# Performance work log

Measured on AMD Instinct MI355X. Metric: run time of the kernel, lower is better.

## Reference

```python
import jax, jax.numpy as jnp
import numpy as np

B, S, D = 4, 2048, 768      # batch, seq_len, embedding_dim
I = 1536                    # inner_dim = embedding_dim * up_proj_factor
H, HD = 8, 64               # num_heads, head_dim
EPS = 1e-5


def setup_inputs() -> dict:
    key = jax.random.key(0)
    ks = jax.random.split(key, 12)
    std = 0.02
    f32 = jnp.float32
    p = {}
    p["x"] = jax.random.normal(ks[0], (B, S, D), f32)
    # block LayerNorm
    p["ln_g"] = jnp.ones((D,), f32)
    p["ln_b"] = jnp.zeros((D,), f32)
    # up / down projections (bias-free, as in the module)
    p["W_up"] = jax.random.normal(ks[1], (D, I), f32) * std
    p["W_down"] = jax.random.normal(ks[2], (I, D), f32) * std
    # mLSTM cell: q/k/v projections to num_heads*head_dim
    p["Wq"] = jax.random.normal(ks[3], (I, H * HD), f32) * std
    p["Wk"] = jax.random.normal(ks[4], (I, H * HD), f32) * std
    p["Wv"] = jax.random.normal(ks[5], (I, H * HD), f32) * std
    # scalar per-head input / forget gate pre-activations
    p["Wi"] = jax.random.normal(ks[6], (I, H), f32) * std
    p["bi"] = jnp.zeros((H,), f32)
    p["Wf"] = jax.random.normal(ks[7], (I, H), f32) * std
    p["bf"] = 3.0 * jnp.ones((H,), f32)  # positive forget-gate bias init
    # output gate and cell output projection
    p["Wo"] = jax.random.normal(ks[8], (I, H * HD), f32) * std
    p["bo"] = jnp.zeros((H * HD,), f32)
    p["mh_g"] = jnp.ones((H, HD), f32)  # per-head norm scale (group norm)
    p["W_out"] = jax.random.normal(ks[9], (H * HD, I), f32) * std
    return p


def _forward(x, ln_g, ln_b, W_up, Wq, Wk, Wv, Wi, bi, Wf, bf, Wo, bo, mh_g, W_out, W_down):
    resid = x
    # LayerNorm
    mu = x.mean(-1, keepdims=True)
    var = ((x - mu) ** 2).mean(-1, keepdims=True)
    h = (x - mu) * jax.lax.rsqrt(var + EPS) * ln_g + ln_b
    # up projection
    u = h @ W_up                                    # (B,S,I)
    # mLSTM projections
    q = (u @ Wq).reshape(B, S, H, HD)
    k = (u @ Wk).reshape(B, S, H, HD) * (HD ** -0.5)
    v = (u @ Wv).reshape(B, S, H, HD)
    i_raw = u @ Wi + bi                             # (B,S,H)
    f_raw = u @ Wf + bf                             # (B,S,H)

    def step(carry, inp):
        C, n, m = carry                             # C:(B,H,HD,HD) n:(B,H,HD) m:(B,H)
        qt, kt, vt, it, ft = inp
        # log-space stabilization of exponential gates
        m_new = jnp.maximum(ft + m, it)
        ig = jnp.exp(it - m_new)
        fg = jnp.exp(ft + m - m_new)
        C = fg[..., None, None] * C + ig[..., None, None] * (vt[..., :, None] * kt[..., None, :])
        n = fg[..., None] * n + ig[..., None] * kt
        num = jnp.einsum('bhvk,bhk->bhv', C, qt)
        den = jnp.maximum(jnp.abs(jnp.einsum('bhk,bhk->bh', n, qt)), 1.0)
        return (C, n, m_new), num / den[..., None]

    xs = (jnp.moveaxis(q, 1, 0), jnp.moveaxis(k, 1, 0), jnp.moveaxis(v, 1, 0),
          jnp.moveaxis(i_raw, 1, 0), jnp.moveaxis(f_raw, 1, 0))
    C0 = jnp.zeros((B, H, HD, HD), x.dtype)
    n0 = jnp.zeros((B, H, HD), x.dtype)
    m0 = jnp.zeros((B, H), x.dtype)
    _, hts = jax.lax.scan(step, (C0, n0, m0), xs)   # (S,B,H,HD)
    ht = jnp.moveaxis(hts, 0, 1)                    # (B,S,H,HD)
    # per-head normalization (group norm, scale only)
    mu2 = ht.mean(-1, keepdims=True)
    var2 = ((ht - mu2) ** 2).mean(-1, keepdims=True)
    hn = (ht - mu2) * jax.lax.rsqrt(var2 + EPS) * mh_g
    # output gate + cell output projection
    o = jax.nn.sigmoid(u @ Wo + bo).reshape(B, S, H, HD)
    y = (o * hn).reshape(B, S, H * HD) @ W_out      # (B,S,I)
    # down projection + residual (dropout=0 -> identity)
    return resid + y @ W_down


def reference(x, ln_g, ln_b, W_up, Wq, Wk, Wv, Wi, bi, Wf, bf, Wo, bo, mh_g, W_out, W_down):
    return _forward(x, ln_g, ln_b, W_up, Wq, Wk, Wv, Wi, bi, Wf, bf, Wo, bo, mh_g, W_out, W_down)
```

## Files before the change

kernel.cpp:

```cpp
#include <hip/hip_runtime.h>
#include <hip/hip_bf16.h>
#include <stdint.h>
#include <stddef.h>

typedef __bf16 bf16_t;
typedef __bf16 bf16x4 __attribute__((ext_vector_type(4)));
typedef __bf16 bf16x8 __attribute__((ext_vector_type(8)));
typedef float  f32x4  __attribute__((ext_vector_type(4)));

#define Bsz  4
#define Ssz  2048
#define Dsz  768
#define Isz  1536
#define Hn   8
#define HDsz 64
#define NTOK (Bsz*Ssz)
#define Lc   64
#define NCH  (Ssz/Lc)
#define NBH  (Bsz*Hn)

#define OFF_H      ((size_t)0)
#define OFF_WQX    ((size_t)12582912)
#define OFF_WQC    ((size_t)18874368)
#define OFF_WDOWNT ((size_t)22020096)
#define OFF_WOC    ((size_t)24379392)
#define OFF_WUPB   ((size_t)25165824)
#define OFF_WUIF   ((size_t)27525120)
#define OFF_BIAS   ((size_t)27549696)
#define OFF_WOUTB  ((size_t)27553792)
#define OFF_QKVO   ((size_t)29126656)
#define OFF_KT     ((size_t)62681088)
#define OFF_VT     ((size_t)71069696)
#define OFF_GATED  ((size_t)79458304)
#define OFF_G      ((size_t)87846912)
#define OFF_IFB    ((size_t)96235520)
#define OFF_BLOC   ((size_t)96759808)
#define OFF_MHAT   ((size_t)97021952)
#define OFF_MST    ((size_t)97284096)
#define OFF_DEC    ((size_t)97288192)
#define OFF_MEND   ((size_t)97292288)
#define OFF_NG     ((size_t)97296384)
#define OFF_NST    ((size_t)97558528)
#define OFF_WOCP   OFF_H
#define OFF_CSTB   OFF_H
#define OFF_COMPP  OFF_QKVO

__device__ __forceinline__ void gload16(const void* gsrc, void* ldst) {
  __builtin_amdgcn_global_load_lds(
      (const __attribute__((address_space(1))) void*)gsrc,
      (__attribute__((address_space(3))) void*)ldst, 16, 0, 0);
}

__device__ __forceinline__ float blockReduceSum256(float v) {
  #pragma unroll
  for (int o = 1; o < 64; o <<= 1) v += __shfl_xor(v, o, 64);
  __shared__ float sh[4];
  int wid = threadIdx.x >> 6;
  __syncthreads();
  if ((threadIdx.x & 63) == 0) sh[wid] = v;
  __syncthreads();
  return sh[0] + sh[1] + sh[2] + sh[3];
}

__global__ __launch_bounds__(256) void prep_weights(
    const float* __restrict__ W_up, const float* __restrict__ Wq,
    const float* __restrict__ Wk, const float* __restrict__ Wv,
    const float* __restrict__ Wo, const float* __restrict__ W_down,
    const float* __restrict__ W_out, const float* __restrict__ bo,
    const float* __restrict__ bi, const float* __restrict__ bfv,
    bf16_t* __restrict__ wqxT, bf16_t* __restrict__ wdownT,
    bf16_t* __restrict__ woutB, bf16_t* __restrict__ wupB,
    float* __restrict__ biasA) {
  __shared__ float tile[32][33];
  const int bid = blockIdx.x;
  const int tx = threadIdx.x, ty = threadIdx.y;
  const float* src; bf16_t* dst; int K, N, bx, by; float scale = 1.f;
  if (bid < 768)       { int l = bid;        src = Wq;     dst = wqxT;                      K = 1536; N = 512; bx = l % 16; by = l / 16; }
  else if (bid < 1536) { int l = bid - 768;  src = Wk;     dst = wqxT + (size_t)512 * Isz;  K = 1536; N = 512; bx = l % 16; by = l / 16; scale = 0.125f; }
  else if (bid < 2304) { int l = bid - 1536; src = Wv;     dst = wqxT + (size_t)1024 * Isz; K = 1536; N = 512; bx = l % 16; by = l / 16; }
  else if (bid < 3072) { int l = bid - 2304; src = Wo;     dst = wqxT + (size_t)1536 * Isz; K = 1536; N = 512; bx = l % 16; by = l / 16; }
  else if (bid < 4224) { int l = bid - 3072; src = W_down; dst = wdownT;                    K = 1536; N = 768; bx = l % 24; by = l / 24; }
  else if (bid < 4992) {
    int base = (bid - 4224) * 1024 + (ty * 32 + tx) * 4;
    #pragma unroll
    for (int e = 0; e < 4; ++e) woutB[base + e] = (bf16_t)W_out[base + e];
    return;
  } else if (bid < 6144) {
    int base = (bid - 4992) * 1024 + (ty * 32 + tx) * 4;
    #pragma unroll
    for (int e = 0; e < 4; ++e) wupB[base + e] = (bf16_t)W_up[base + e];
    return;
  } else {
    int tid = ty * 32 + tx;
    for (int i = tid; i < 528; i += 256)
      biasA[i] = (i < 512) ? bo[i] : ((i < 520) ? bi[i - 512] : bfv[i - 520]);
    return;
  }
  int n0 = bx * 32, k0 = by * 32;
  #pragma unroll
  for (int j = 0; j < 32; j += 8)
    tile[ty + j][tx] = src[(size_t)(k0 + ty + j) * N + n0 + tx];
  __syncthreads();
  #pragma unroll
  for (int j = 0; j < 32; j += 8)
    dst[(size_t)(n0 + ty + j) * K + k0 + tx] = (bf16_t)(tile[tx][ty + j] * scale);
}

__global__ __launch_bounds__(64) void build_wuif(const float* __restrict__ W_up,
                                                 const float* __restrict__ Wi,
                                                 const float* __restrict__ Wf,
                                                 bf16_t* __restrict__ dst ) {
  int d = blockIdx.x;
  int lane = threadIdx.x;
  float acc[16];
  #pragma unroll
  for (int j = 0; j < 16; ++j) acc[j] = 0.f;
  for (int i = lane; i < Isz; i += 64) {
    float w = W_up[(size_t)d * Isz + i];
    f32x4 wi0 = *(const f32x4*)&Wi[(size_t)i * 8];
    f32x4 wi1 = *(const f32x4*)&Wi[(size_t)i * 8 + 4];
    f32x4 wf0 = *(const f32x4*)&Wf[(size_t)i * 8];
    f32x4 wf1 = *(const f32x4*)&Wf[(size_t)i * 8 + 4];
    #pragma unroll
    for (int j = 0; j < 4; ++j) {
      acc[j]      += w * wi0[j];
      acc[4 + j]  += w * wi1[j];
      acc[8 + j]  += w * wf0[j];
      acc[12 + j] += w * wf1[j];
    }
  }
  #pragma unroll
  for (int j = 0; j < 16; ++j)
    #pragma unroll
    for (int o = 1; o < 64; o <<= 1) acc[j] += __shfl_xor(acc[j], o, 64);
  if (lane == 0) {
    #pragma unroll
    for (int j = 0; j < 16; ++j)
      dst[(size_t)j * Dsz + d] = (bf16_t)acc[j];
  }
}

__global__ __launch_bounds__(256) void gemm_partk(const bf16_t* __restrict__ A,
                                                  const bf16_t* __restrict__ Bt,
                                                  float* __restrict__ P,
                                                  int M, int N, int Ktot, int kslice) {
  __shared__ bf16_t As[128 * 64];
  __shared__ bf16_t Bs[128 * 64];
  const int t = threadIdx.x;
  const int w = t >> 6, l = t & 63;
  const int tile_m = blockIdx.y * 128, tile_n = blockIdx.x * 128;
  const int kz = blockIdx.z;
  const int wr = w >> 1, wc = w & 1;
  const int lrow = l >> 3;
  const int lks = ((l & 7) * 8) ^ (lrow << 3);
  const int l15 = l & 15, l4 = l >> 4;

  f32x4 acc[4][4];
  #pragma unroll
  for (int m = 0; m < 4; ++m)
    #pragma unroll
    for (int n = 0; n < 4; ++n) acc[m][n] = (f32x4){0.f, 0.f, 0.f, 0.f};

  for (int k0 = kz * kslice; k0 < kz * kslice + kslice; k0 += 64) {
    #pragma unroll
    for (int i = 0; i < 4; ++i) {
      int ch = w * 4 + i;
      int row = ch * 8 + lrow;
      gload16(A  + (size_t)(tile_m + row) * Ktot + k0 + lks, &As[ch * 512]);
      gload16(Bt + (size_t)(tile_n + row) * Ktot + k0 + lks, &Bs[ch * 512]);
    }
    __syncthreads();
    #pragma unroll
    for (int kk = 0; kk < 2; ++kk) {
      bf16x8 af[4], bfr[4];
      #pragma unroll
      for (int m = 0; m < 4; ++m) {
        int r = wr * 64 + m * 16 + l15;
        af[m] = *(const bf16x8*)&As[r * 64 + ((kk * 32 + l4 * 8) ^ ((r & 7) << 3))];
      }
      #pragma unroll
      for (int n = 0; n < 4; ++n) {
        int r = wc * 64 + n * 16 + l15;
        bfr[n] = *(const bf16x8*)&Bs[r * 64 + ((kk * 32 + l4 * 8) ^ ((r & 7) << 3))];
      }
      #pragma unroll
      for (int m = 0; m < 4; ++m)
        #pragma unroll
        for (int n = 0; n < 4; ++n)
          acc[m][n] = __builtin_amdgcn_mfma_f32_16x16x32_bf16(af[m], bfr[n], acc[m][n], 0, 0, 0);
    }
    __syncthreads();
  }

  const int rbase = tile_m + wr * 64 + l4 * 4;
  const int cbase = tile_n + wc * 64 + l15;
  float* Pz = P + (size_t)kz * M * N;
  #pragma unroll
  for (int m = 0; m < 4; ++m)
    #pragma unroll
    for (int n = 0; n < 4; ++n)
      #pragma unroll
      for (int j = 0; j < 4; ++j)
        Pz[(size_t)(rbase + m * 16 + j) * N + cbase + n * 16] = acc[m][n][j];
}

__global__ __launch_bounds__(256) void partk_reduce(const float* __restrict__ P,
                                                    bf16_t* __restrict__ out,
                                                    int nelem, int nz) {
  int i = blockIdx.x * 256 + threadIdx.x;
  if (i < nelem) {
    float s = 0.f;
    for (int z = 0; z < nz; ++z) s += P[(size_t)z * nelem + i];
    out[i] = (bf16_t)s;
  }
}

__global__ __launch_bounds__(256) void ln_kernel(const float* __restrict__ x,
                                                 const float* __restrict__ g,
                                                 const float* __restrict__ bta,
                                                 bf16_t* __restrict__ h) {
  size_t tok = blockIdx.x;
  const float* xr = x + tok * Dsz;
  int t = threadIdx.x;
  float v[3]; float s = 0.f;
  #pragma unroll
  for (int i = 0; i < 3; ++i) { v[i] = xr[t + 256 * i]; s += v[i]; }
  s = blockReduceSum256(s);
  float mu = s * (1.f / Dsz);
  float s2 = 0.f;
  #pragma unroll
  for (int i = 0; i < 3; ++i) { float d = v[i] - mu; s2 += d * d; }
  s2 = blockReduceSum256(s2);
  float rs = rsqrtf(s2 * (1.f / Dsz) + 1e-5f);
  #pragma unroll
  for (int i = 0; i < 3; ++i) {
    int col = t + 256 * i;
    h[tok * Dsz + col] = (bf16_t)((v[i] - mu) * rs * g[col] + bta[col]);
  }
}

__global__ __launch_bounds__(256) void ifproj_mfma(const bf16_t* __restrict__ h,
                                                   const bf16_t* __restrict__ wuifT,
                                                   const float* __restrict__ bi,
                                                   const float* __restrict__ bfv,
                                                   float* __restrict__ ifb) {
  __shared__ bf16_t As[128 * 64];
  __shared__ bf16_t Bs[16 * 64];
  const int t = threadIdx.x, w = t >> 6, l = t & 63;
  const int l15 = l & 15, l4 = l >> 4;
  const int lrow = l >> 3, lk = (l & 7) * 8;
  const int tile_m = blockIdx.x * 128;
  f32x4 acc[2];
  acc[0] = (f32x4){0.f, 0.f, 0.f, 0.f};
  acc[1] = (f32x4){0.f, 0.f, 0.f, 0.f};

  for (int k0 = 0; k0 < Dsz; k0 += 64) {
    #pragma unroll
    for (int i = 0; i < 4; ++i) {
      int ch = w * 4 + i;
      int row = ch * 8 + lrow;
      gload16(h + (size_t)(tile_m + row) * Dsz + k0 + lk, &As[ch * 512]);
    }
    if (t < 128) {
      int rr = t >> 3, c0 = (t & 7) * 8;
      *(bf16x8*)&Bs[rr * 64 + c0] = *(const bf16x8*)(wuifT + (size_t)rr * Dsz + k0 + c0);
    }
    __syncthreads();
    #pragma unroll
    for (int kk = 0; kk < 2; ++kk) {
      bf16x8 bfr = *(const bf16x8*)&Bs[l15 * 64 + kk * 32 + l4 * 8];
      #pragma unroll
      for (int m = 0; m < 2; ++m) {
        bf16x8 af = *(const bf16x8*)&As[(w * 32 + m * 16 + l15) * 64 + kk * 32 + l4 * 8];
        acc[m] = __builtin_amdgcn_mfma_f32_16x16x32_bf16(af, bfr, acc[m], 0, 0, 0);
      }
    }
    __syncthreads();
  }
  float bias = (l15 < 8) ? bi[l15] : bfv[l15 - 8];
  #pragma unroll
  for (int m = 0; m < 2; ++m)
    #pragma unroll
    for (int j = 0; j < 4; ++j) {
      int row = tile_m + w * 32 + m * 16 + l4 * 4 + j;
      ifb[(size_t)row * 16 + l15] = acc[m][j] + bias;
    }
}

template<int EPI>
__global__ __launch_bounds__(512, 4) void gemm_mn(const bf16_t* __restrict__ A,
                                                  const bf16_t* __restrict__ Bt,
                                                  void* __restrict__ Cout,
                                                  const void* __restrict__ extra,
                                                  bf16_t* __restrict__ kTg,
                                                  bf16_t* __restrict__ vTg,
                                                  int M, int N, int K) {
  __shared__ bf16_t As[256 * 64];
  __shared__ bf16_t Bs[128 * 64];
  const int t = threadIdx.x;
  const int w = t >> 6, l = t & 63;
  const int wm = w >> 1, wn = w & 1;
  const int l15 = l & 15, l4 = l >> 4;

  const int gx = gridDim.x;
  const int nwg = gx * gridDim.y;
  const int cpx = nwg >> 3;
  int bid = blockIdx.y * gx + blockIdx.x;
  int wg = (bid & 7) * cpx + (bid >> 3);
  const int tile_m = (wg / gx) * 256;
  const int tile_n = (wg % gx) * 128;

  f32x4 acc[4][4];
  #pragma unroll
  for (int m = 0; m < 4; ++m)
    #pragma unroll
    for (int n = 0; n < 4; ++n) acc[m][n] = (f32x4){0.f, 0.f, 0.f, 0.f};

  for (int k0 = 0; k0 < K; k0 += 64) {
    #pragma unroll
    for (int j = 0; j < 4; ++j) {
      int c = t + j * 512;
      int row = c >> 3;
      int ec = ((c & 7) * 8) ^ ((row & 7) << 3);
      gload16(A + (size_t)(tile_m + row) * K + k0 + ec, (char*)As + (size_t)c * 16);
    }
    #pragma unroll
    for (int j = 0; j < 2; ++j) {
      int c = t + j * 512;
      int row = c >> 3;
      int ec = ((c & 7) * 8) ^ ((row & 7) << 3);
      gload16(Bt + (size_t)(tile_n + row) * K + k0 + ec, (char*)Bs + (size_t)c * 16);
    }
    __syncthreads();
    #pragma unroll
    for (int kk = 0; kk < 2; ++kk) {
      bf16x8 aF[4], bF[4];
      #pragma unroll
      for (int m = 0; m < 4; ++m) {
        int r = wm * 64 + m * 16 + l15;
        aF[m] = *(const bf16x8*)((const char*)As + r * 128 + ((kk * 64 + l4 * 16) ^ ((r & 7) << 4)));
      }
      #pragma unroll
      for (int n = 0; n < 4; ++n) {
        int r = wn * 64 + n * 16 + l15;
        bF[n] = *(const bf16x8*)((const char*)Bs + r * 128 + ((kk * 64 + l4 * 16) ^ ((r & 7) << 4)));
      }
      #pragma unroll
      for (int m = 0; m < 4; ++m)
        #pragma unroll
        for (int n = 0; n < 4; ++n)
          acc[m][n] = __builtin_amdgcn_mfma_f32_16x16x32_bf16(aF[m], bF[n], acc[m][n], 0, 0, 0);
    }
    __syncthreads();
  }

  const int rbase = tile_m + wm * 64 + l4 * 4;
  const int cbase = tile_n + wn * 64 + l15;
  if constexpr (EPI == 5) {
    const float* bias = (const float*)extra;
    #pragma unroll
    for (int m = 0; m < 4; ++m) {
      int row0 = rbase + m * 16;
      int bb = row0 >> 11, s0 = row0 & 2047;
      #pragma unroll
      for (int n = 0; n < 4; ++n) {
        int col = cbase + n * 16;
        if (col < 512) {
          #pragma unroll
          for (int j = 0; j < 4; ++j)
            ((bf16_t*)Cout)[(size_t)(row0 + j) * 2048 + col] = (bf16_t)acc[m][n][j];
        } else if (col < 1024) {
          int hd = col - 512;
          bf16x4 pk;
          #pragma unroll
          for (int j = 0; j < 4; ++j) {
            bf16_t bv = (bf16_t)acc[m][n][j];
            ((bf16_t*)Cout)[(size_t)(row0 + j) * 2048 + col] = bv;
            pk[j] = bv;
          }
          *(bf16x4*)(kTg + ((size_t)(bb * 8 + (hd >> 6)) * 64 + (hd & 63)) * Ssz + s0) = pk;
        } else if (col < 1536) {
          int hd = col - 1024;
          bf16x4 pv;
          #pragma unroll
          for (int j = 0; j < 4; ++j) pv[j] = (bf16_t)acc[m][n][j];
          *(bf16x4*)(vTg + ((size_t)(bb * 8 + (hd >> 6)) * 64 + (hd & 63)) * Ssz + s0) = pv;
        } else {
          float b = bias[col - 1536];
          #pragma unroll
          for (int j = 0; j < 4; ++j) {
            float z = acc[m][n][j] + b;
            ((bf16_t*)Cout)[(size_t)(row0 + j) * 2048 + col] = (bf16_t)(1.f / (1.f + __expf(-z)));
          }
        }
      }
    }
  } else {
    #pragma unroll
    for (int m = 0; m < 4; ++m)
      #pragma unroll
      for (int n = 0; n < 4; ++n)
        #pragma unroll
        for (int j = 0; j < 4; ++j) {
          int row = rbase + m * 16 + j;
          int col = cbase + n * 16;
          ((float*)Cout)[(size_t)row * N + col] =
              acc[m][n][j] + ((const float*)extra)[(size_t)row * N + col];
        }
  }
}

__global__ __launch_bounds__(64) void gates_a(const float* __restrict__ ifb,
                                              float* __restrict__ blocal,
                                              float* __restrict__ Mhat) {
  int bh = blockIdx.x >> 5, c = blockIdx.x & 31;
  int b = bh >> 3, h = bh & 7;
  int lane = threadIdx.x;
  size_t tok = (size_t)b * Ssz + c * Lc + lane;
  float iv = ifb[tok * 16 + h];
  float fv = ifb[tok * 16 + 8 + h];
  float bt = fv;
  #pragma unroll
  for (int d = 1; d < 64; d <<= 1) { float o = __shfl_up(bt, d, 64); if (lane >= d) bt += o; }
  float a = iv - bt;
  float pm = a;
  #pragma unroll
  for (int d = 1; d < 64; d <<= 1) { float o = __shfl_up(pm, d, 64); if (lane >= d) pm = fmaxf(pm, o); }
  blocal[(size_t)bh * Ssz + c * Lc + lane] = bt;
  Mhat[(size_t)bh * Ssz + c * Lc + lane] = bt + pm;
}

__global__ void gates_b(const float* __restrict__ blocal, const float* __restrict__ Mhat,
                        float* __restrict__ mstart, float* __restrict__ decays,
                        float* __restrict__ mend) {
  int bh = threadIdx.x;
  if (bh < NBH) {
    float M = 0.f;
    for (int c = 0; c < NCH; ++c) {
      mstart[bh * NCH + c] = M;
      float bL = blocal[(size_t)bh * Ssz + c * Lc + 63];
      float Mh = Mhat[(size_t)bh * Ssz + c * Lc + 63];
      float Mn = fmaxf(M + bL, Mh);
      decays[bh * NCH + c] = __expf(M + bL - Mn);
      mend[bh * NCH + c] = Mn;
      M = Mn;
    }
  }
}

__global__ __launch_bounds__(256) void chunk_inc_mfma(const bf16_t* __restrict__ kTg,
                                                      const bf16_t* __restrict__ vTg,
                                                      const float* __restrict__ ifb,
                                                      const float* __restrict__ blocal,
                                                      const float* __restrict__ mend,
                                                      bf16_t* __restrict__ G,
                                                      float* __restrict__ ng) {
  int bh = blockIdx.x >> 5, c = blockIdx.x & 31;
  int b = bh >> 3, h = bh & 7;
  __shared__ bf16_t Vt[64 * 64];
  __shared__ bf16_t Kw[64 * 64];
  __shared__ float wsh[64];
  const int t = threadIdx.x, w = t >> 6, l = t & 63;
  const int l15 = l & 15, l4 = l >> 4;
  if (t < 64) {
    float mL = mend[bh * NCH + c];
    float bL = blocal[(size_t)bh * Ssz + c * Lc + 63];
    float bt = blocal[(size_t)bh * Ssz + c * Lc + t];
    float iv = ifb[((size_t)b * Ssz + c * Lc + t) * 16 + h];
    wsh[t] = __expf(iv + bL - bt - mL);
  }
  __syncthreads();
  {
    const int r = l >> 3, c8 = (l & 7) * 8;
    #pragma unroll
    for (int i = 0; i < 2; ++i) {
      int seg = w * 2 + i, row = seg * 8 + r;
      gload16(vTg + ((size_t)bh * 64 + row) * Ssz + c * 64 + c8, &Vt[seg * 512]);
    }
    #pragma unroll
    for (int i = 0; i < 2; ++i) {
      int e = t + i * 256; int row = e >> 3, c0 = (e & 7) * 8;
      bf16x8 kv = *(const bf16x8*)(kTg + ((size_t)bh * 64 + row) * Ssz + c * 64 + c0);
      #pragma unroll
      for (int j = 0; j < 8; ++j) kv[j] = (bf16_t)((float)kv[j] * wsh[c0 + j]);
      *(bf16x8*)&Kw[row * 64 + c0] = kv;
    }
  }
  __syncthreads();
  f32x4 acc[4];
  #pragma unroll
  for (int n = 0; n < 4; ++n) acc[n] = (f32x4){0.f, 0.f, 0.f, 0.f};
  #pragma unroll
  for (int kk = 0; kk < 2; ++kk) {
    bf16x8 af = *(const bf16x8*)&Vt[(w * 16 + l15) * 64 + kk * 32 + l4 * 8];
    #pragma unroll
    for (int n = 0; n < 4; ++n) {
      bf16x8 bfr = *(const bf16x8*)&Kw[(n * 16 + l15) * 64 + kk * 32 + l4 * 8];
      acc[n] = __builtin_amdgcn_mfma_f32_16x16x32_bf16(af, bfr, acc[n], 0, 0, 0);
    }
  }
  size_t gb = ((size_t)bh * NCH + c) * 4096;
  #pragma unroll
  for (int n = 0; n < 4; ++n)
    #pragma unroll
    for (int j = 0; j < 4; ++j) {
      int row = w * 16 + l4 * 4 + j;
      int col = n * 16 + l15;
      G[gb + (size_t)row * 64 + col] = (bf16_t)acc[n][j];
    }
  if (t < 64) {
    float s = 0.f;
    for (int s2 = 0; s2 < 64; ++s2) s += (float)Kw[t * 64 + s2];
    ng[((size_t)bh * NCH + c) * 64 + t] = s;
  }
}

__global__ __launch_bounds__(256) void state_scan(const bf16_t* __restrict__ G,
                                                  const float* __restrict__ ng,
                                                  const float* __restrict__ decays,
                                                  bf16_t* __restrict__ CstB,
                                                  float* __restrict__ nst) {
  int gid = blockIdx.x;
  if (gid < 512) {
    int idx = gid * 256 + threadIdx.x;
    int bh = idx >> 12, e = idx & 4095;
    const float* d = decays + bh * NCH;
    float C = 0.f;
    #pragma unroll
    for (int c = 0; c < NCH; ++c) {
      size_t o = ((size_t)bh * NCH + c) * 4096 + e;
      CstB[o] = (bf16_t)C;
      C = d[c] * C + (float)G[o];
    }
  } else {
    int idx = (gid - 512) * 256 + threadIdx.x;
    int bh = idx >> 6, e = idx & 63;
    const float* d = decays + bh * NCH;
    float n = 0.f;
    #pragma unroll
    for (int c = 0; c < NCH; ++c) {
      size_t o = ((size_t)bh * NCH + c) * 64 + e;
      nst[o] = n;
      n = d[c] * n + ng[o];
    }
  }
}

__global__ __launch_bounds__(256) void intra_mfma(const bf16_t* __restrict__ qkvo,
                                                  const bf16_t* __restrict__ vTg,
                                                  const bf16_t* __restrict__ CstB,
                                                  const float* __restrict__ nst,
                                                  const float* __restrict__ ifb,
                                                  const float* __restrict__ blocal,
                                                  const float* __restrict__ Mhat,
                                                  const float* __restrict__ mstart,
                                                  const float* __restrict__ mhg,
                                                  bf16_t* __restrict__ gated) {
  int bh = blockIdx.x >> 5, c = blockIdx.x & 31;
  int b = bh >> 3, h = bh & 7;
  __shared__ bf16_t qs[64 * 64];
  __shared__ bf16_t ks[64 * 64];
  __shared__ bf16_t vTs[64 * 64];
  __shared__ bf16_t Cs[64 * 64];
  __shared__ float nin[64], den_s[64], ssrc[64], sdst[64], esc[64];
  const int t = threadIdx.x, w = t >> 6, l = t & 63;
  const int l15 = l & 15, l4 = l >> 4;
  const size_t tok0 = (size_t)b * Ssz + c * Lc;
  const size_t cbase = ((size_t)bh * NCH + c) * 4096;

  if (t < 64) {
    nin[t] = nst[((size_t)bh * NCH + c) * 64 + t];
    float bt = blocal[(size_t)bh * Ssz + c * Lc + t];
    float Mh2 = Mhat[(size_t)bh * Ssz + c * Lc + t];
    float Mc = mstart[bh * NCH + c];
    float iv = ifb[(tok0 + t) * 16 + h];
    float mt = fmaxf(Mc + bt, Mh2);
    ssrc[t] = iv - bt;
    sdst[t] = bt - mt;
    esc[t]  = __expf(Mc + bt - mt);
  }
  {
    const int r = l >> 3, c8 = (l & 7) * 8;
    #pragma unroll
    for (int i = 0; i < 2; ++i) {
      int seg = w * 2 + i, row = seg * 8 + r;
      gload16(qkvo + (tok0 + row) * 2048 + h * 64 + c8,          &qs[seg * 512]);
      gload16(qkvo + (tok0 + row) * 2048 + 512 + h * 64 + c8,    &ks[seg * 512]);
      gload16(vTg + ((size_t)bh * 64 + row) * Ssz + c * 64 + c8, &vTs[seg * 512]);
      gload16(CstB + cbase + seg * 512 + l * 8,                  &Cs[seg * 512]);
    }
  }
  __syncthreads();

  f32x4 aS[4];
  #pragma unroll
  for (int n = 0; n < 4; ++n) aS[n] = (f32x4){0.f, 0.f, 0.f, 0.f};
  #pragma unroll
  for (int kk = 0; kk < 2; ++kk) {
    bf16x8 af = *(const bf16x8*)&qs[(w * 16 + l15) * 64 + kk * 32 + l4 * 8];
    #pragma unroll
    for (int n = 0; n < 4; ++n) {
      bf16x8 bfr = *(const bf16x8*)&ks[(n * 16 + l15) * 64 + kk * 32 + l4 * 8];
      aS[n] = __builtin_amdgcn_mfma_f32_16x16x32_bf16(af, bfr, aS[n], 0, 0, 0);
    }
  }
  {
    int row = w * 16 + (l >> 2);
    int c0 = (l & 3) * 16;
    float e = esc[row];
    #pragma unroll
    for (int i2 = 0; i2 < 2; ++i2) {
      bf16x8 v8 = *(const bf16x8*)&qs[row * 64 + c0 + i2 * 8];
      #pragma unroll
      for (int j = 0; j < 8; ++j) v8[j] = (bf16_t)((float)v8[j] * e);
      *(bf16x8*)&qs[row * 64 + c0 + i2 * 8] = v8;
    }
  }
  float rs[4] = {0.f, 0.f, 0.f, 0.f};
  #pragma unroll
  for (int n = 0; n < 4; ++n) {
    int col = n * 16 + l15;
    float es = ssrc[col];
    #pragma unroll
    for (int j = 0; j < 4; ++j) {
      int row = w * 16 + l4 * 4 + j;
      float p = (col <= row) ? aS[n][j] * __expf(es + sdst[row]) : 0.f;
      aS[n][j] = p;
      rs[j] += p;
    }
  }
  #pragma unroll
  for (int j = 0; j < 4; ++j) {
    rs[j] += __shfl_xor(rs[j], 1, 64);
    rs[j] += __shfl_xor(rs[j], 2, 64);
    rs[j] += __shfl_xor(rs[j], 4, 64);
    rs[j] += __shfl_xor(rs[j], 8, 64);
  }
  if (l15 == 0) {
    #pragma unroll
    for (int j = 0; j < 4; ++j) den_s[w * 16 + l4 * 4 + j] = rs[j];
  }
  __syncthreads();

  #pragma unroll
  for (int n = 0; n < 4; ++n)
    #pragma unroll
    for (int j = 0; j < 4; ++j)
      ks[(w * 16 + l4 * 4 + j) * 64 + n * 16 + l15] = (bf16_t)aS[n][j];

  {
    int row = w * 16 + (l >> 2);
    int c0 = (l & 3) * 16;
    float part = 0.f;
    #pragma unroll
    for (int i2 = 0; i2 < 16; ++i2)
      part += (float)qs[row * 64 + c0 + i2] * nin[c0 + i2];
    part += __shfl_xor(part, 1, 64);
    part += __shfl_xor(part, 2, 64);
    if ((l & 3) == 0)
      den_s[row] = fmaxf(fabsf(den_s[row] + part), 1.0f);
  }
  __syncthreads();

  f32x4 aO[4];
  #pragma unroll
  for (int n = 0; n < 4; ++n) aO[n] = (f32x4){0.f, 0.f, 0.f, 0.f};
  #pragma unroll
  for (int kk = 0; kk < 2; ++kk) {
    bf16x8 afP = *(const bf16x8*)&ks[(w * 16 + l15) * 64 + kk * 32 + l4 * 8];
    bf16x8 afQ = *(const bf16x8*)&qs[(w * 16 + l15) * 64 + kk * 32 + l4 * 8];
    #pragma unroll
    for (int n = 0; n < 4; ++n) {
      bf16x8 bV = *(const bf16x8*)&vTs[(n * 16 + l15) * 64 + kk * 32 + l4 * 8];
      bf16x8 bC = *(const bf16x8*)&Cs[(n * 16 + l15) * 64 + kk * 32 + l4 * 8];
      aO[n] = __builtin_amdgcn_mfma_f32_16x16x32_bf16(afP, bV, aO[n], 0, 0, 0);
      aO[n] = __builtin_amdgcn_mfma_f32_16x16x32_bf16(afQ, bC, aO[n], 0, 0, 0);
    }
  }

  #pragma unroll
  for (int j = 0; j < 4; ++j) {
    int row = w * 16 + l4 * 4 + j;
    float rinv = 1.f / den_s[row];
    float ov[4];
    #pragma unroll
    for (int n = 0; n < 4; ++n) ov[n] = aO[n][j] * rinv;
    float s = ov[0] + ov[1] + ov[2] + ov[3];
    s += __shfl_xor(s, 1, 64); s += __shfl_xor(s, 2, 64);
    s += __shfl_xor(s, 4, 64); s += __shfl_xor(s, 8, 64);
    float mu = s * (1.f / 64.f);
    float s2 = 0.f;
    #pragma unroll
    for (int n = 0; n < 4; ++n) { float d = ov[n] - mu; s2 += d * d; }
    s2 += __shfl_xor(s2, 1, 64); s2 += __shfl_xor(s2, 2, 64);
    s2 += __shfl_xor(s2, 4, 64); s2 += __shfl_xor(s2, 8, 64);
    float rstd = rsqrtf(s2 * (1.f / 64.f) + 1e-5f);
    size_t tok = tok0 + row;
    #pragma unroll
    for (int n = 0; n < 4; ++n) {
      int colh = n * 16 + l15;
      float og = (float)qkvo[tok * 2048 + 1536 + h * 64 + colh];
      float hn = (ov[n] - mu) * rstd * mhg[h * 64 + colh];
      gated[tok * 512 + h * 64 + colh] = (bf16_t)(og * hn);
    }
  }
}

extern "C" void kernel_launch(void* const* d_in, const int* in_sizes, int n_in,
                              void* d_out, int out_size, void* d_ws, size_t ws_size,
                              hipStream_t stream) {
  const float* x     = (const float*)d_in[0];
  const float* ln_g  = (const float*)d_in[1];
  const float* ln_b  = (const float*)d_in[2];
  const float* W_up  = (const float*)d_in[3];
  const float* W_down= (const float*)d_in[4];
  const float* Wq    = (const float*)d_in[5];
  const float* Wk    = (const float*)d_in[6];
  const float* Wv    = (const float*)d_in[7];
  const float* Wi    = (const float*)d_in[8];
  const float* bi    = (const float*)d_in[9];
  const float* Wf    = (const float*)d_in[10];
  const float* bfv   = (const float*)d_in[11];
  const float* Wo    = (const float*)d_in[12];
  const float* bo    = (const float*)d_in[13];
  const float* mh_g  = (const float*)d_in[14];
  const float* W_out = (const float*)d_in[15];

  char* ws = (char*)d_ws;
  bf16_t* hbuf   = (bf16_t*)(ws + OFF_H);
  bf16_t* wqxT   = (bf16_t*)(ws + OFF_WQX);
  bf16_t* wqcT   = (bf16_t*)(ws + OFF_WQC);
  bf16_t* wdownT = (bf16_t*)(ws + OFF_WDOWNT);
  bf16_t* wocT   = (bf16_t*)(ws + OFF_WOC);
  bf16_t* wupB   = (bf16_t*)(ws + OFF_WUPB);
  bf16_t* wuifT  = (bf16_t*)(ws + OFF_WUIF);
  float*  biasA  = (float*)(ws + OFF_BIAS);
  bf16_t* woutB  = (bf16_t*)(ws + OFF_WOUTB);
  bf16_t* qkvob  = (bf16_t*)(ws + OFF_QKVO);
  bf16_t* kTg    = (bf16_t*)(ws + OFF_KT);
  bf16_t* vTg    = (bf16_t*)(ws + OFF_VT);
  bf16_t* gbuf   = (bf16_t*)(ws + OFF_GATED);
  bf16_t* Gbuf   = (bf16_t*)(ws + OFF_G);
  float*  ifb    = (float*)(ws + OFF_IFB);
  float*  bloc   = (float*)(ws + OFF_BLOC);
  float*  Mh     = (float*)(ws + OFF_MHAT);
  float*  mst    = (float*)(ws + OFF_MST);
  float*  decays = (float*)(ws + OFF_DEC);
  float*  mendb  = (float*)(ws + OFF_MEND);
  float*  ngbuf  = (float*)(ws + OFF_NG);
  float*  nst    = (float*)(ws + OFF_NST);
  float*  wocP   = (float*)(ws + OFF_WOCP);
  float*  compP  = (float*)(ws + OFF_COMPP);
  bf16_t* CstB   = (bf16_t*)(ws + OFF_CSTB);

  prep_weights<<<6145, dim3(32, 8), 0, stream>>>(W_up, Wq, Wk, Wv, Wo, W_down, W_out,
                                                 bo, bi, bfv, wqxT, wdownT, woutB, wupB, biasA);
  build_wuif<<<Dsz, 64, 0, stream>>>(W_up, Wi, Wf, wuifT);

  gemm_partk<<<dim3(6, 16, 4), 256, 0, stream>>>(wqxT, wupB, compP, 2048, 768, 1536, 384);
  partk_reduce<<<6144, 256, 0, stream>>>(compP, wqcT, 2048 * 768, 4);
  gemm_partk<<<dim3(4, 6, 8), 256, 0, stream>>>(wdownT, woutB, wocP, 768, 512, 1536, 192);
  partk_reduce<<<1536, 256, 0, stream>>>(wocP, wocT, 768 * 512, 8);

  ln_kernel<<<NTOK, 256, 0, stream>>>(x, ln_g, ln_b, hbuf);
  ifproj_mfma<<<NTOK / 128, 256, 0, stream>>>(hbuf, wuifT, bi, bfv, ifb);

  gemm_mn<5><<<dim3(2048 / 128, NTOK / 256), 512, 0, stream>>>(hbuf, wqcT, qkvob, biasA, kTg, vTg, NTOK, 2048, Dsz);

  gates_a<<<NBH * NCH, 64, 0, stream>>>(ifb, bloc, Mh);
  gates_b<<<1, 32, 0, stream>>>(bloc, Mh, mst, decays, mendb);
  chunk_inc_mfma<<<NBH * NCH, 256, 0, stream>>>(kTg, vTg, ifb, bloc, mendb, Gbuf, ngbuf);
  state_scan<<<520, 256, 0, stream>>>(Gbuf, ngbuf, decays, CstB, nst);
  intra_mfma<<<NBH * NCH, 256, 0, stream>>>(qkvob, vTg, CstB, nst, ifb, bloc, Mh, mst, mh_g, gbuf);

  gemm_mn<3><<<dim3(Dsz / 128, NTOK / 256), 512, 0, stream>>>(gbuf, wocT, (float*)d_out, x, nullptr, nullptr, NTOK, Dsz, 512);
}
```

Measured before the change: 163.2 us.

## Merge small launches and vectorize reductions and state scan

Folds build_wuif into prep_weights, combines the two split-K weight GEMMs into one launch and their reductions into one vectorized kernel, and fuses gates_a/gates_b into one per-head kernel. It also vectorizes state_scan to four elements per thread. The aim is fewer kernel launches and serial tails, plus wider memory accesses. In exchange, state_scan runs fewer blocks (136), which lowers parallelism, and the fused gates kernel runs only 32 blocks.

```diff
diff --git a/kernel.cpp b/kernel.cpp
--- a/kernel.cpp
+++ b/kernel.cpp
@@ -66,14 +66,16 @@
     const float* __restrict__ W_up, const float* __restrict__ Wq,
     const float* __restrict__ Wk, const float* __restrict__ Wv,
     const float* __restrict__ Wo, const float* __restrict__ W_down,
-    const float* __restrict__ W_out, const float* __restrict__ bo,
+    const float* __restrict__ W_out, const float* __restrict__ Wi,
+    const float* __restrict__ Wf, const float* __restrict__ bo,
     const float* __restrict__ bi, const float* __restrict__ bfv,
     bf16_t* __restrict__ wqxT, bf16_t* __restrict__ wdownT,
     bf16_t* __restrict__ woutB, bf16_t* __restrict__ wupB,
-    float* __restrict__ biasA) {
+    bf16_t* __restrict__ wuifT, float* __restrict__ biasA) {
   __shared__ float tile[32][33];
   const int bid = blockIdx.x;
   const int tx = threadIdx.x, ty = threadIdx.y;
+  const int tid = ty * 32 + tx;
   const float* src; bf16_t* dst; int K, N, bx, by; float scale = 1.f;
   if (bid < 768)       { int l = bid;        src = Wq;     dst = wqxT;                      K = 1536; N = 512; bx = l % 16; by = l / 16; }
   else if (bid < 1536) { int l = bid - 768;  src = Wk;     dst = wqxT + (size_t)512 * Isz;  K = 1536; N = 512; bx = l % 16; by = l / 16; scale = 0.125f; }
@@ -81,17 +83,46 @@
   else if (bid < 3072) { int l = bid - 2304; src = Wo;     dst = wqxT + (size_t)1536 * Isz; K = 1536; N = 512; bx = l % 16; by = l / 16; }
   else if (bid < 4224) { int l = bid - 3072; src = W_down; dst = wdownT;                    K = 1536; N = 768; bx = l % 24; by = l / 24; }
   else if (bid < 4992) {
-    int base = (bid - 4224) * 1024 + (ty * 32 + tx) * 4;
+    int base = (bid - 4224) * 1024 + tid * 4;
     #pragma unroll
     for (int e = 0; e < 4; ++e) woutB[base + e] = (bf16_t)W_out[base + e];
     return;
   } else if (bid < 6144) {
-    int base = (bid - 4992) * 1024 + (ty * 32 + tx) * 4;
+    int base = (bid - 4992) * 1024 + tid * 4;
     #pragma unroll
     for (int e = 0; e < 4; ++e) wupB[base + e] = (bf16_t)W_up[base + e];
     return;
+  } else if (bid < 6336) {
+    int sub = tid >> 6, lane = tid & 63;
+    int d = (bid - 6144) * 4 + sub;
+    float acc[16];
+    #pragma unroll
+    for (int j = 0; j < 16; ++j) acc[j] = 0.f;
+    for (int i = lane; i < Isz; i += 64) {
+      float w = W_up[(size_t)d * Isz + i];
+      f32x4 wi0 = *(const f32x4*)&Wi[(size_t)i * 8];
+      f32x4 wi1 = *(const f32x4*)&Wi[(size_t)i * 8 + 4];
+      f32x4 wf0 = *(const f32x4*)&Wf[(size_t)i * 8];
+      f32x4 wf1 = *(const f32x4*)&Wf[(size_t)i * 8 + 4];
+      #pragma unroll
+      for (int j = 0; j < 4; ++j) {
+        acc[j]      += w * wi0[j];
+        acc[4 + j]  += w * wi1[j];
+        acc[8 + j]  += w * wf0[j];
+        acc[12 + j] += w * wf1[j];
+      }
+    }
+    #pragma unroll
+    for (int j = 0; j < 16; ++j)
+      #pragma unroll
+      for (int o = 1; o < 64; o <<= 1) acc[j] += __shfl_xor(acc[j], o, 64);
+    if (lane == 0) {
+      #pragma unroll
+      for (int j = 0; j < 16; ++j)
+        wuifT[(size_t)j * Dsz + d] = (bf16_t)acc[j];
+    }
+    return;
   } else {
-    int tid = ty * 32 + tx;
     for (int i = tid; i < 528; i += 256)
       biasA[i] = (i < 512) ? bo[i] : ((i < 520) ? bi[i - 512] : bfv[i - 520]);
     return;
@@ -106,50 +137,30 @@
     dst[(size_t)(n0 + ty + j) * K + k0 + tx] = (bf16_t)(tile[tx][ty + j] * scale);
 }
 
-__global__ __launch_bounds__(64) void build_wuif(const float* __restrict__ W_up,
-                                                 const float* __restrict__ Wi,
-                                                 const float* __restrict__ Wf,
-                                                 bf16_t* __restrict__ dst ) {
-  int d = blockIdx.x;
-  int lane = threadIdx.x;
-  float acc[16];
-  #pragma unroll
-  for (int j = 0; j < 16; ++j) acc[j] = 0.f;
-  for (int i = lane; i < Isz; i += 64) {
-    float w = W_up[(size_t)d * Isz + i];
-    f32x4 wi0 = *(const f32x4*)&Wi[(size_t)i * 8];
-    f32x4 wi1 = *(const f32x4*)&Wi[(size_t)i * 8 + 4];
-    f32x4 wf0 = *(const f32x4*)&Wf[(size_t)i * 8];
-    f32x4 wf1 = *(const f32x4*)&Wf[(size_t)i * 8 + 4];
-    #pragma unroll
-    for (int j = 0; j < 4; ++j) {
-      acc[j]      += w * wi0[j];
-      acc[4 + j]  += w * wi1[j];
-      acc[8 + j]  += w * wf0[j];
-      acc[12 + j] += w * wf1[j];
-    }
-  }
-  #pragma unroll
-  for (int j = 0; j < 16; ++j)
-    #pragma unroll
-    for (int o = 1; o < 64; o <<= 1) acc[j] += __shfl_xor(acc[j], o, 64);
-  if (lane == 0) {
-    #pragma unroll
-    for (int j = 0; j < 16; ++j)
-      dst[(size_t)j * Dsz + d] = (bf16_t)acc[j];
-  }
-}
-
-__global__ __launch_bounds__(256) void gemm_partk(const bf16_t* __restrict__ A,
-                                                  const bf16_t* __restrict__ Bt,
-                                                  float* __restrict__ P,
-                                                  int M, int N, int Ktot, int kslice) {
+__global__ __launch_bounds__(256) void gemm_partk2(const bf16_t* __restrict__ wqxT,
+                                                   const bf16_t* __restrict__ wupB,
+                                                   float* __restrict__ compP,
+                                                   const bf16_t* __restrict__ wdownT,
+                                                   const bf16_t* __restrict__ woutB,
+                                                   float* __restrict__ wocP) {
+  const bf16_t *A, *Bt; float* P;
+  int M, N, Ktot, kslice, bx, by, kz;
+  int bid = blockIdx.x;
+  if (bid < 384) {
+    A = wqxT; Bt = wupB; P = compP;
+    M = 2048; N = 768; Ktot = 1536; kslice = 384;
+    kz = bid / 96; int r = bid % 96; by = r / 6; bx = r % 6;
+  } else {
+    int l = bid - 384;
+    A = wdownT; Bt = woutB; P = wocP;
+    M = 768; N = 512; Ktot = 1536; kslice = 192;
+    kz = l / 24; int r = l % 24; by = r / 4; bx = r % 4;
+  }
   __shared__ bf16_t As[128 * 64];
   __shared__ bf16_t Bs[128 * 64];
   const int t = threadIdx.x;
   const int w = t >> 6, l = t & 63;
-  const int tile_m = blockIdx.y * 128, tile_n = blockIdx.x * 128;
-  const int kz = blockIdx.z;
+  const int tile_m = by * 128, tile_n = bx * 128;
   const int wr = w >> 1, wc = w & 1;
   const int lrow = l >> 3;
   const int lks = ((l & 7) * 8) ^ (lrow << 3);
@@ -204,15 +215,23 @@
         Pz[(size_t)(rbase + m * 16 + j) * N + cbase + n * 16] = acc[m][n][j];
 }
 
-__global__ __launch_bounds__(256) void partk_reduce(const float* __restrict__ P,
-                                                    bf16_t* __restrict__ out,
-                                                    int nelem, int nz) {
-  int i = blockIdx.x * 256 + threadIdx.x;
-  if (i < nelem) {
-    float s = 0.f;
-    for (int z = 0; z < nz; ++z) s += P[(size_t)z * nelem + i];
-    out[i] = (bf16_t)s;
-  }
+__global__ __launch_bounds__(256) void reduce2(const float* __restrict__ compP,
+                                               bf16_t* __restrict__ wqcT,
+                                               const float* __restrict__ wocP,
+                                               bf16_t* __restrict__ wocT) {
+  int bid = blockIdx.x;
+  const float* P; bf16_t* out; int nelem, nz, e;
+  if (bid < 1536) { P = compP; out = wqcT; nelem = 2048 * 768; nz = 4; e = (bid * 256 + threadIdx.x) * 4; }
+  else            { P = wocP;  out = wocT; nelem = 768 * 512;  nz = 8; e = ((bid - 1536) * 256 + threadIdx.x) * 4; }
+  f32x4 s = {0.f, 0.f, 0.f, 0.f};
+  for (int z = 0; z < nz; ++z) {
+    f32x4 v = *(const f32x4*)&P[(size_t)z * nelem + e];
+    s[0] += v[0]; s[1] += v[1]; s[2] += v[2]; s[3] += v[3];
+  }
+  bf16x4 ov;
+  #pragma unroll
+  for (int j = 0; j < 4; ++j) ov[j] = (bf16_t)s[j];
+  *(bf16x4*)&out[e] = ov;
 }
 
 __global__ __launch_bounds__(256) void ln_kernel(const float* __restrict__ x,
@@ -410,38 +429,38 @@
   }
 }
 
-__global__ __launch_bounds__(64) void gates_a(const float* __restrict__ ifb,
-                                              float* __restrict__ blocal,
-                                              float* __restrict__ Mhat) {
-  int bh = blockIdx.x >> 5, c = blockIdx.x & 31;
+__global__ __launch_bounds__(256) void gates_fused(const float* __restrict__ ifb,
+                                                   float* __restrict__ blocal,
+                                                   float* __restrict__ Mhat,
+                                                   float* __restrict__ mstart,
+                                                   float* __restrict__ decays,
+                                                   float* __restrict__ mend) {
+  int bh = blockIdx.x;
   int b = bh >> 3, h = bh & 7;
-  int lane = threadIdx.x;
-  size_t tok = (size_t)b * Ssz + c * Lc + lane;
-  float iv = ifb[tok * 16 + h];
-  float fv = ifb[tok * 16 + 8 + h];
-  float bt = fv;
-  #pragma unroll
-  for (int d = 1; d < 64; d <<= 1) { float o = __shfl_up(bt, d, 64); if (lane >= d) bt += o; }
-  float a = iv - bt;
-  float pm = a;
-  #pragma unroll
-  for (int d = 1; d < 64; d <<= 1) { float o = __shfl_up(pm, d, 64); if (lane >= d) pm = fmaxf(pm, o); }
-  blocal[(size_t)bh * Ssz + c * Lc + lane] = bt;
-  Mhat[(size_t)bh * Ssz + c * Lc + lane] = bt + pm;
-}
-
-__global__ void gates_b(const float* __restrict__ blocal, const float* __restrict__ Mhat,
-                        float* __restrict__ mstart, float* __restrict__ decays,
-                        float* __restrict__ mend) {
-  int bh = threadIdx.x;
-  if (bh < NBH) {
+  int wid = threadIdx.x >> 6, lane = threadIdx.x & 63;
+  __shared__ float bL_s[32], Mh_s[32];
+  for (int c = wid; c < NCH; c += 4) {
+    size_t tok = (size_t)b * Ssz + c * Lc + lane;
+    float iv = ifb[tok * 16 + h];
+    float fv = ifb[tok * 16 + 8 + h];
+    float bt = fv;
+    #pragma unroll
+    for (int d = 1; d < 64; d <<= 1) { float o = __shfl_up(bt, d, 64); if (lane >= d) bt += o; }
+    float a = iv - bt;
+    float pm = a;
+    #pragma unroll
+    for (int d = 1; d < 64; d <<= 1) { float o = __shfl_up(pm, d, 64); if (lane >= d) pm = fmaxf(pm, o); }
+    blocal[(size_t)bh * Ssz + c * Lc + lane] = bt;
+    Mhat[(size_t)bh * Ssz + c * Lc + lane] = bt + pm;
+    if (lane == 63) { bL_s[c] = bt; Mh_s[c] = bt + pm; }
+  }
+  __syncthreads();
+  if (threadIdx.x == 0) {
     float M = 0.f;
     for (int c = 0; c < NCH; ++c) {
       mstart[bh * NCH + c] = M;
-      float bL = blocal[(size_t)bh * Ssz + c * Lc + 63];
-      float Mh = Mhat[(size_t)bh * Ssz + c * Lc + 63];
-      float Mn = fmaxf(M + bL, Mh);
-      decays[bh * NCH + c] = __expf(M + bL - Mn);
+      float Mn = fmaxf(M + bL_s[c], Mh_s[c]);
+      decays[bh * NCH + c] = __expf(M + bL_s[c] - Mn);
       mend[bh * NCH + c] = Mn;
       M = Mn;
     }
@@ -521,19 +540,26 @@
                                                   bf16_t* __restrict__ CstB,
                                                   float* __restrict__ nst) {
   int gid = blockIdx.x;
-  if (gid < 512) {
-    int idx = gid * 256 + threadIdx.x;
-    int bh = idx >> 12, e = idx & 4095;
+  if (gid < 128) {
+    int e4 = (gid * 256 + threadIdx.x) * 4;
+    int bh = e4 >> 12, e = e4 & 4095;
     const float* d = decays + bh * NCH;
-    float C = 0.f;
+    float C0 = 0.f, C1 = 0.f, C2 = 0.f, C3 = 0.f;
     #pragma unroll
     for (int c = 0; c < NCH; ++c) {
       size_t o = ((size_t)bh * NCH + c) * 4096 + e;
-      CstB[o] = (bf16_t)C;
-      C = d[c] * C + (float)G[o];
+      bf16x4 st;
+      st[0] = (bf16_t)C0; st[1] = (bf16_t)C1; st[2] = (bf16_t)C2; st[3] = (bf16_t)C3;
+      *(bf16x4*)&CstB[o] = st;
+      bf16x4 g4 = *(const bf16x4*)&G[o];
+      float dc = d[c];
+      C0 = dc * C0 + (float)g4[0];
+      C1 = dc * C1 + (float)g4[1];
+      C2 = dc * C2 + (float)g4[2];
+      C3 = dc * C3 + (float)g4[3];
     }
   } else {
-    int idx = (gid - 512) * 256 + threadIdx.x;
+    int idx = (gid - 128) * 256 + threadIdx.x;
     int bh = idx >> 6, e = idx & 63;
     const float* d = decays + bh * NCH;
     float n = 0.f;
@@ -753,24 +779,20 @@
   float*  compP  = (float*)(ws + OFF_COMPP);
   bf16_t* CstB   = (bf16_t*)(ws + OFF_CSTB);
 
-  prep_weights<<<6145, dim3(32, 8), 0, stream>>>(W_up, Wq, Wk, Wv, Wo, W_down, W_out,
-                                                 bo, bi, bfv, wqxT, wdownT, woutB, wupB, biasA);
-  build_wuif<<<Dsz, 64, 0, stream>>>(W_up, Wi, Wf, wuifT);
-
-  gemm_partk<<<dim3(6, 16, 4), 256, 0, stream>>>(wqxT, wupB, compP, 2048, 768, 1536, 384);
-  partk_reduce<<<6144, 256, 0, stream>>>(compP, wqcT, 2048 * 768, 4);
-  gemm_partk<<<dim3(4, 6, 8), 256, 0, stream>>>(wdownT, woutB, wocP, 768, 512, 1536, 192);
-  partk_reduce<<<1536, 256, 0, stream>>>(wocP, wocT, 768 * 512, 8);
+  prep_weights<<<6337, dim3(32, 8), 0, stream>>>(W_up, Wq, Wk, Wv, Wo, W_down, W_out,
+                                                 Wi, Wf, bo, bi, bfv,
+                                                 wqxT, wdownT, woutB, wupB, wuifT, biasA);
+  gemm_partk2<<<576, 256, 0, stream>>>(wqxT, wupB, compP, wdownT, woutB, wocP);
+  reduce2<<<1920, 256, 0, stream>>>(compP, wqcT, wocP, wocT);
 
   ln_kernel<<<NTOK, 256, 0, stream>>>(x, ln_g, ln_b, hbuf);
   ifproj_mfma<<<NTOK / 128, 256, 0, stream>>>(hbuf, wuifT, bi, bfv, ifb);
 
   gemm_mn<5><<<dim3(2048 / 128, NTOK / 256), 512, 0, stream>>>(hbuf, wqcT, qkvob, biasA, kTg, vTg, NTOK, 2048, Dsz);
 
-  gates_a<<<NBH * NCH, 64, 0, stream>>>(ifb, bloc, Mh);
-  gates_b<<<1, 32, 0, stream>>>(bloc, Mh, mst, decays, mendb);
+  gates_fused<<<NBH, 256, 0, stream>>>(ifb, bloc, Mh, mst, decays, mendb);
   chunk_inc_mfma<<<NBH * NCH, 256, 0, stream>>>(kTg, vTg, ifb, bloc, mendb, Gbuf, ngbuf);
-  state_scan<<<520, 256, 0, stream>>>(Gbuf, ngbuf, decays, CstB, nst);
+  state_scan<<<136, 256, 0, stream>>>(Gbuf, ngbuf, decays, CstB, nst);
   intra_mfma<<<NBH * NCH, 256, 0, stream>>>(qkvob, vTg, CstB, nst, ifb, bloc, Mh, mst, mh_g, gbuf);
 
   gemm_mn<3><<<dim3(Dsz / 128, NTOK / 256), 512, 0, stream>>>(gbuf, wocT, (float*)d_out, x, nullptr, nullptr, NTOK, Dsz, 512);
```

New measurement: 157.5 us. 3.5% less time.
